# Performance work log

Hardware: AMD Instinct MI355X
Metric: run time of the kernel (lower is better)

Reference implementation:

```python
import jax, jax.numpy as jnp
import numpy as np

B, H, W, P, F = 2, 192, 320, 128, 8  # batch, image height, image width, points/ray, feat dim


def setup_inputs() -> dict:
    key = jax.random.key(0)
    k1, k2, k3 = jax.random.split(key, 3)
    rays_densities = jax.random.uniform(k1, (B, H, W, P, 1), dtype=jnp.float32)  # in [0,1]
    rays_features = jax.random.normal(k2, (B, H, W, P, F), dtype=jnp.float32)
    # monotone-ish positive depths along each ray
    lengths = jax.random.uniform(k3, (B, H, W, P), dtype=jnp.float32) * 50.0
    return {
        "rays_densities": rays_densities,
        "rays_features": rays_features,
        "lengths": lengths,
    }


def reference(rays_densities, rays_features, lengths):
    # wall=True: force furthest sample density to 1 so probs sum to 1
    d = rays_densities[..., 0].at[..., -1].set(1.0)  # (B,H,W,P)
    # cumulative density, clamped to 1, then per-sample absorption prob via diff
    cum = jnp.minimum(jnp.cumsum(d, axis=-1), 1.0)
    zeros = jnp.zeros(cum.shape[:-1] + (1,), cum.dtype)
    probs = jnp.diff(cum, axis=-1, prepend=zeros)  # (B,H,W,P)
    # expected depth and expected features along each ray
    depth = jnp.sum(probs * lengths, axis=-1)  # (B,H,W)
    features = jnp.sum(probs[..., None] * rays_features, axis=-2)  # (B,H,W,F)
    return depth, features
```

## Files before the change

kernel.cpp:

```cpp
#include <hip/hip_runtime.h>
#include <hip/hip_bf16.h>


#define RM_P 128
#define RM_F 8

__global__ __launch_bounds__(256) void DepthEmissionRaymarcher_9904194584773_kernel(
    const float* __restrict__ dens,
    const float* __restrict__ feat,
    const float* __restrict__ len,
    float* __restrict__ out_depth,
    float* __restrict__ out_feat,
    int n_rays)
{
    int ray = blockIdx.x * blockDim.x + threadIdx.x;
    if (ray >= n_rays) return;

    const float4* d4 = (const float4*)(dens + (long)ray * RM_P);
    const float4* l4 = (const float4*)(len  + (long)ray * RM_P);
    const float4* fr = (const float4*)(feat + (long)ray * RM_P * RM_F);

    float  depth = 0.0f;
    float4 acc0  = make_float4(0.f, 0.f, 0.f, 0.f);
    float4 acc1  = make_float4(0.f, 0.f, 0.f, 0.f);
    float  cum   = 0.0f;

    {
        float4 dv = d4[0];
        float4 lv = l4[0];
        float4 f0a = fr[0], f0b = fr[1];
        float4 f1a = fr[2], f1b = fr[3];
        float4 f2a = fr[4], f2b = fr[5];
        float4 f3a = fr[6], f3b = fr[7];

        float c0 = fminf(dv.x,            1.0f);
        float c1 = fminf(c0 + dv.y,       1.0f);
        float c2 = fminf(c1 + dv.z,       1.0f);
        float c3 = fminf(c2 + dv.w,       1.0f);
        float p0 = c0;
        float p1 = c1 - c0;
        float p2 = c2 - c1;
        float p3 = c3 - c2;
        cum = c3;

        depth = p0*lv.x + p1*lv.y + p2*lv.z + p3*lv.w;

        acc0.x = p0*f0a.x + p1*f1a.x + p2*f2a.x + p3*f3a.x;
        acc0.y = p0*f0a.y + p1*f1a.y + p2*f2a.y + p3*f3a.y;
        acc0.z = p0*f0a.z + p1*f1a.z + p2*f2a.z + p3*f3a.z;
        acc0.w = p0*f0a.w + p1*f1a.w + p2*f2a.w + p3*f3a.w;
        acc1.x = p0*f0b.x + p1*f1b.x + p2*f2b.x + p3*f3b.x;
        acc1.y = p0*f0b.y + p1*f1b.y + p2*f2b.y + p3*f3b.y;
        acc1.z = p0*f0b.z + p1*f1b.z + p2*f2b.z + p3*f3b.z;
        acc1.w = p0*f0b.w + p1*f1b.w + p2*f2b.w + p3*f3b.w;
    }

    #pragma unroll 1
    for (int b = 1; b < RM_P / 4; ++b) {
        if (cum >= 1.0f) break;

        float4 dv = d4[b];
        float4 lv = l4[b];
        if (b == RM_P / 4 - 1) dv.w = 1.0f;

        float4 fa0 = fr[8*b + 0], fb0 = fr[8*b + 1];
        float4 fa1 = fr[8*b + 2], fb1 = fr[8*b + 3];
        float4 fa2 = fr[8*b + 4], fb2 = fr[8*b + 5];
        float4 fa3 = fr[8*b + 6], fb3 = fr[8*b + 7];

        float c0 = fminf(cum + dv.x, 1.0f);
        float c1 = fminf(c0  + dv.y, 1.0f);
        float c2 = fminf(c1  + dv.z, 1.0f);
        float c3 = fminf(c2  + dv.w, 1.0f);
        float p0 = c0 - cum;
        float p1 = c1 - c0;
        float p2 = c2 - c1;
        float p3 = c3 - c2;
        cum = c3;

        depth += p0*lv.x + p1*lv.y + p2*lv.z + p3*lv.w;

        acc0.x += p0*fa0.x + p1*fa1.x + p2*fa2.x + p3*fa3.x;
        acc0.y += p0*fa0.y + p1*fa1.y + p2*fa2.y + p3*fa3.y;
        acc0.z += p0*fa0.z + p1*fa1.z + p2*fa2.z + p3*fa3.z;
        acc0.w += p0*fa0.w + p1*fa1.w + p2*fa2.w + p3*fa3.w;
        acc1.x += p0*fb0.x + p1*fb1.x + p2*fb2.x + p3*fb3.x;
        acc1.y += p0*fb0.y + p1*fb1.y + p2*fb2.y + p3*fb3.y;
        acc1.z += p0*fb0.z + p1*fb1.z + p2*fb2.z + p3*fb3.z;
        acc1.w += p0*fb0.w + p1*fb1.w + p2*fb2.w + p3*fb3.w;
    }

    out_depth[ray] = depth;
    float4* of = (float4*)(out_feat + (long)ray * RM_F);
    of[0] = acc0;
    of[1] = acc1;
}

extern "C" void kernel_launch(void* const* d_in, const int* in_sizes, int n_in,
                              void* d_out, int out_size, void* d_ws, size_t ws_size,
                              hipStream_t stream) {
    const float* dens = (const float*)d_in[0];
    const float* feat = (const float*)d_in[1];
    const float* len  = (const float*)d_in[2];

    const int n_rays = in_sizes[2] / RM_P;

    float* out_depth = (float*)d_out;
    float* out_feat  = out_depth + n_rays;

    dim3 block(256);
    dim3 grid((n_rays + 255) / 256);
    DepthEmissionRaymarcher_9904194584773_kernel<<<grid, block, 0, stream>>>(
        dens, feat, len, out_depth, out_feat, n_rays);
}
```

Measured before the change: 590.3 us.

## Batch ray sample loads and shrink blocks to 64 threads

Loads the first eight samples at once, processes the middle of each ray in groups of sixteen samples with all loads issued before compute, and peels the last eight samples to apply the wall density. Block size drops to 64 with a launch bound allowing two waves per SIMD. The goal is more memory-level parallelism per thread. The cost is fetching extra data past the early-termination point and higher register pressure.

After: 593.0 us. No clear change (+0.5%).

```diff
diff --git a/kernel.cpp b/kernel.cpp
--- a/kernel.cpp
+++ b/kernel.cpp
@@ -5,7 +5,26 @@
 #define RM_P 128
 #define RM_F 8
 
-__global__ __launch_bounds__(256) void DepthEmissionRaymarcher_9904194584773_kernel(
+#define RM_BATCH4(DVv, LVv, Fv)                                              \
+  do {                                                                       \
+    float c0 = fminf(cum + (DVv).x, 1.0f);                                   \
+    float c1 = fminf(c0  + (DVv).y, 1.0f);                                   \
+    float c2 = fminf(c1  + (DVv).z, 1.0f);                                   \
+    float c3 = fminf(c2  + (DVv).w, 1.0f);                                   \
+    float p0 = c0 - cum, p1 = c1 - c0, p2 = c2 - c1, p3 = c3 - c2;           \
+    cum = c3;                                                                \
+    depth += p0*(LVv).x + p1*(LVv).y + p2*(LVv).z + p3*(LVv).w;              \
+    acc0.x += p0*(Fv)[0].x + p1*(Fv)[2].x + p2*(Fv)[4].x + p3*(Fv)[6].x;     \
+    acc0.y += p0*(Fv)[0].y + p1*(Fv)[2].y + p2*(Fv)[4].y + p3*(Fv)[6].y;     \
+    acc0.z += p0*(Fv)[0].z + p1*(Fv)[2].z + p2*(Fv)[4].z + p3*(Fv)[6].z;     \
+    acc0.w += p0*(Fv)[0].w + p1*(Fv)[2].w + p2*(Fv)[4].w + p3*(Fv)[6].w;     \
+    acc1.x += p0*(Fv)[1].x + p1*(Fv)[3].x + p2*(Fv)[5].x + p3*(Fv)[7].x;     \
+    acc1.y += p0*(Fv)[1].y + p1*(Fv)[3].y + p2*(Fv)[5].y + p3*(Fv)[7].y;     \
+    acc1.z += p0*(Fv)[1].z + p1*(Fv)[3].z + p2*(Fv)[5].z + p3*(Fv)[7].z;     \
+    acc1.w += p0*(Fv)[1].w + p1*(Fv)[3].w + p2*(Fv)[5].w + p3*(Fv)[7].w;     \
+  } while (0)
+
+__global__ __launch_bounds__(64, 2) void DepthEmissionRaymarcher_9904194584773_kernel(
     const float* __restrict__ dens,
     const float* __restrict__ feat,
     const float* __restrict__ len,
@@ -26,68 +45,44 @@
     float  cum   = 0.0f;
 
     {
-        float4 dv = d4[0];
-        float4 lv = l4[0];
-        float4 f0a = fr[0], f0b = fr[1];
-        float4 f1a = fr[2], f1b = fr[3];
-        float4 f2a = fr[4], f2b = fr[5];
-        float4 f3a = fr[6], f3b = fr[7];
+        float4 DV0 = d4[0], DV1 = d4[1];
+        float4 LV0 = l4[0], LV1 = l4[1];
+        float4 FP[16];
+        #pragma unroll
+        for (int k = 0; k < 16; ++k) FP[k] = fr[k];
 
-        float c0 = fminf(dv.x,            1.0f);
-        float c1 = fminf(c0 + dv.y,       1.0f);
-        float c2 = fminf(c1 + dv.z,       1.0f);
-        float c3 = fminf(c2 + dv.w,       1.0f);
-        float p0 = c0;
-        float p1 = c1 - c0;
-        float p2 = c2 - c1;
-        float p3 = c3 - c2;
-        cum = c3;
-
-        depth = p0*lv.x + p1*lv.y + p2*lv.z + p3*lv.w;
-
-        acc0.x = p0*f0a.x + p1*f1a.x + p2*f2a.x + p3*f3a.x;
-        acc0.y = p0*f0a.y + p1*f1a.y + p2*f2a.y + p3*f3a.y;
-        acc0.z = p0*f0a.z + p1*f1a.z + p2*f2a.z + p3*f3a.z;
-        acc0.w = p0*f0a.w + p1*f1a.w + p2*f2a.w + p3*f3a.w;
-        acc1.x = p0*f0b.x + p1*f1b.x + p2*f2b.x + p3*f3b.x;
-        acc1.y = p0*f0b.y + p1*f1b.y + p2*f2b.y + p3*f3b.y;
-        acc1.z = p0*f0b.z + p1*f1b.z + p2*f2b.z + p3*f3b.z;
-        acc1.w = p0*f0b.w + p1*f1b.w + p2*f2b.w + p3*f3b.w;
+        RM_BATCH4(DV0, LV0, (&FP[0]));
+        RM_BATCH4(DV1, LV1, (&FP[8]));
     }
 
     #pragma unroll 1
-    for (int b = 1; b < RM_P / 4; ++b) {
+    for (int b = 2; b <= 26; b += 4) {
         if (cum >= 1.0f) break;
 
-        float4 dv = d4[b];
-        float4 lv = l4[b];
-        if (b == RM_P / 4 - 1) dv.w = 1.0f;
+        float4 DV[4], LV[4], F[4][8];
+        #pragma unroll
+        for (int u = 0; u < 4; ++u) {
+            DV[u] = d4[b + u];
+            LV[u] = l4[b + u];
+            #pragma unroll
+            for (int k = 0; k < 8; ++k) F[u][k] = fr[8*(b + u) + k];
+        }
+        #pragma unroll
+        for (int u = 0; u < 4; ++u) {
+            RM_BATCH4(DV[u], LV[u], F[u]);
+        }
+    }
 
-        float4 fa0 = fr[8*b + 0], fb0 = fr[8*b + 1];
-        float4 fa1 = fr[8*b + 2], fb1 = fr[8*b + 3];
-        float4 fa2 = fr[8*b + 4], fb2 = fr[8*b + 5];
-        float4 fa3 = fr[8*b + 6], fb3 = fr[8*b + 7];
+    if (cum < 1.0f) {
+        float4 DV0 = d4[30], DV1 = d4[31];
+        float4 LV0 = l4[30], LV1 = l4[31];
+        float4 FT[16];
+        #pragma unroll
+        for (int k = 0; k < 16; ++k) FT[k] = fr[240 + k];
+        DV1.w = 1.0f;
 
-        float c0 = fminf(cum + dv.x, 1.0f);
-        float c1 = fminf(c0  + dv.y, 1.0f);
-        float c2 = fminf(c1  + dv.z, 1.0f);
-        float c3 = fminf(c2  + dv.w, 1.0f);
-        float p0 = c0 - cum;
-        float p1 = c1 - c0;
-        float p2 = c2 - c1;
-        float p3 = c3 - c2;
-        cum = c3;
-
-        depth += p0*lv.x + p1*lv.y + p2*lv.z + p3*lv.w;
-
-        acc0.x += p0*fa0.x + p1*fa1.x + p2*fa2.x + p3*fa3.x;
-        acc0.y += p0*fa0.y + p1*fa1.y + p2*fa2.y + p3*fa3.y;
-        acc0.z += p0*fa0.z + p1*fa1.z + p2*fa2.z + p3*fa3.z;
-        acc0.w += p0*fa0.w + p1*fa1.w + p2*fa2.w + p3*fa3.w;
-        acc1.x += p0*fb0.x + p1*fb1.x + p2*fb2.x + p3*fb3.x;
-        acc1.y += p0*fb0.y + p1*fb1.y + p2*fb2.y + p3*fb3.y;
-        acc1.z += p0*fb0.z + p1*fb1.z + p2*fb2.z + p3*fb3.z;
-        acc1.w += p0*fb0.w + p1*fb1.w + p2*fb2.w + p3*fb3.w;
+        RM_BATCH4(DV0, LV0, (&FT[0]));
+        RM_BATCH4(DV1, LV1, (&FT[8]));
     }
 
     out_depth[ray] = depth;
@@ -108,8 +103,8 @@
     float* out_depth = (float*)d_out;
     float* out_feat  = out_depth + n_rays;
 
-    dim3 block(256);
-    dim3 grid((n_rays + 255) / 256);
+    dim3 block(64);
+    dim3 grid((n_rays + 63) / 64);
     DepthEmissionRaymarcher_9904194584773_kernel<<<grid, block, 0, stream>>>(
         dens, feat, len, out_depth, out_feat, n_rays);
 }
```
